# Kernel optimization log

Hardware: AMD Instinct MI355X
Metric: run time of the kernel (lower is better)

Reference implementation:

```python
import jax, jax.numpy as jnp
import numpy as np

DIM = 1024
NUM_EXPERTS = 8
NUM_SELECTED = 2
HIDDEN = 4096
B, S = 2, 2048


def setup_inputs() -> dict:
    key = jax.random.key(0)
    ks = jax.random.split(key, 12)
    scale = 0.02
    x = jax.random.normal(ks[0], (B, S, DIM), dtype=jnp.float32)
    router_w = jax.random.normal(ks[1], (DIM, NUM_EXPERTS), dtype=jnp.float32) * scale
    router_b = jnp.zeros((NUM_EXPERTS,), dtype=jnp.float32)
    w1 = jax.random.normal(ks[2], (NUM_EXPERTS, DIM, HIDDEN), dtype=jnp.float32) * scale
    b1 = jnp.zeros((NUM_EXPERTS, HIDDEN), dtype=jnp.float32)
    w2 = jax.random.normal(ks[3], (NUM_EXPERTS, HIDDEN, DIM), dtype=jnp.float32) * scale
    b2 = jnp.zeros((NUM_EXPERTS, DIM), dtype=jnp.float32)
    sw1 = jax.random.normal(ks[4], (DIM, HIDDEN), dtype=jnp.float32) * scale
    sb1 = jnp.zeros((HIDDEN,), dtype=jnp.float32)
    sw2 = jax.random.normal(ks[5], (HIDDEN, DIM), dtype=jnp.float32) * scale
    sb2 = jnp.zeros((DIM,), dtype=jnp.float32)
    return {"x": x, "router_w": router_w, "router_b": router_b,
            "w1": w1, "b1": b1, "w2": w2, "b2": b2,
            "sw1": sw1, "sb1": sb1, "sw2": sw2, "sb2": sb2}


def _ffn(x, wa, ba, wb, bb):
    # exact (erf) GELU, matching torch nn.GELU() default
    h = jax.nn.gelu(x @ wa + ba, approximate=False)
    return h @ wb + bb


def reference(x, router_w, router_b, w1, b1, w2, b2, sw1, sb1, sw2, sb2):
    # router: [B,S,E] softmax, then top-k over experts (eval mode: no noise)
    logits = x @ router_w + router_b
    probs = jax.nn.softmax(logits, axis=-1)
    top_w, top_i = jax.lax.top_k(probs, NUM_SELECTED)  # [B,S,K]
    # combine weights per expert: [B,S,E]; masked-out experts get weight 0,
    # so computing every expert densely and weighting is the same math as
    # the original masked-dispatch loop.
    combine = jnp.sum(top_w[..., None] * jax.nn.one_hot(top_i, NUM_EXPERTS, dtype=x.dtype), axis=-2)
    shared = _ffn(x, sw1, sb1, sw2, sb2)
    out = shared
    for e in range(NUM_EXPERTS):  # small fixed structural loop over experts
        out = out + combine[..., e:e + 1] * _ffn(x, w1[e], b1[e], w2[e], b2[e])
    return out
```

## Files before the change

### kernel.cpp

```cpp
#include <hip/hip_runtime.h>
#include <hip/hip_bf16.h>

#define T_TOK   4096
#define DIM     1024
#define NEXP    8
#define HID     4096
#define CAPPAD  9216
#define MTOT    (CAPPAD + T_TOK)
static_assert(MTOT % 128 == 0, "MTOT must be multiple of 128");

typedef __attribute__((ext_vector_type(8))) short bf16x8;
typedef __attribute__((ext_vector_type(4))) float f32x4;

typedef const __attribute__((address_space(1))) unsigned int* gas1_u32;
typedef __attribute__((address_space(3))) unsigned int* las3_u32;

__device__ __forceinline__ void async_ld16(const void* g, void* l) {
    __builtin_amdgcn_global_load_lds((gas1_u32)g, (las3_u32)l, 16, 0, 0);
}

__device__ __forceinline__ unsigned short f2bf(float f) {
    union { float f; unsigned u; } v; v.f = f;
    unsigned r = v.u + 0x7fffu + ((v.u >> 16) & 1u);
    return (unsigned short)(r >> 16);
}

__global__ __launch_bounds__(256)
void router_kernel(const float* __restrict__ x, const float* __restrict__ rw,
                   const float* __restrict__ rb, int* __restrict__ cnt,
                   int* __restrict__ top_e, float* __restrict__ top_w) {
    const int tid  = threadIdx.x;
    const int lane = tid & 63;
    const int t    = blockIdx.x * 4 + (tid >> 6);
    const float* xr = x + (size_t)t * DIM;
    float acc[NEXP];
#pragma unroll
    for (int e = 0; e < NEXP; ++e) acc[e] = 0.f;
    for (int d = lane; d < DIM; d += 64) {
        float xv = xr[d];
        const float* r = rw + (size_t)d * NEXP;
#pragma unroll
        for (int e = 0; e < NEXP; ++e) acc[e] += xv * r[e];
    }
#pragma unroll
    for (int off = 32; off > 0; off >>= 1) {
#pragma unroll
        for (int e = 0; e < NEXP; ++e) acc[e] += __shfl_down(acc[e], off);
    }
    if (lane == 0) {
        float lg[NEXP], p[NEXP];
        float mx = -1e30f;
#pragma unroll
        for (int e = 0; e < NEXP; ++e) { lg[e] = acc[e] + rb[e]; mx = fmaxf(mx, lg[e]); }
        float s = 0.f;
#pragma unroll
        for (int e = 0; e < NEXP; ++e) { p[e] = expf(lg[e] - mx); s += p[e]; }
        float inv = 1.f / s;
#pragma unroll
        for (int e = 0; e < NEXP; ++e) p[e] *= inv;
        int i1 = 0;
#pragma unroll
        for (int e = 1; e < NEXP; ++e) if (p[e] > p[i1]) i1 = e;
        int i2 = (i1 == 0) ? 1 : 0;
#pragma unroll
        for (int e = 0; e < NEXP; ++e) if (e != i1 && p[e] > p[i2]) i2 = e;
        top_e[2 * t]     = i1;  top_w[2 * t]     = p[i1];
        top_e[2 * t + 1] = i2;  top_w[2 * t + 1] = p[i2];
        atomicAdd(&cnt[i1], 1);
        atomicAdd(&cnt[i2], 1);
    }
}

__global__ void offsets_kernel(const int* __restrict__ cnt, int* __restrict__ poff) {
    if (threadIdx.x == 0) {
        int acc = 0;
#pragma unroll
        for (int e = 0; e < NEXP; ++e) { poff[e] = acc; acc += (cnt[e] + 127) & ~127; }
        poff[NEXP] = acc;
    }
}

__global__ __launch_bounds__(256)
void assign_kernel(const int* __restrict__ top_e, const int* __restrict__ poff,
                   int* __restrict__ cursor, int* __restrict__ slot_of,
                   int* __restrict__ rowtok) {
    int t = blockIdx.x * 256 + threadIdx.x;
#pragma unroll
    for (int k = 0; k < 2; ++k) {
        int e = top_e[2 * t + k];
        int s = poff[e] + atomicAdd(&cursor[e], 1);
        slot_of[2 * t + k] = s;
        rowtok[s] = t;
    }
}

__global__ __launch_bounds__(256)
void gather_kernel(const float* __restrict__ x, const int* __restrict__ rowtok,
                   unsigned short* __restrict__ xg) {
    int row = blockIdx.x;
    int t = (row >= CAPPAD) ? (row - CAPPAD) : rowtok[row];
    ushort4* dst = (ushort4*)(xg + (size_t)row * DIM) + threadIdx.x;
    if (t < 0) { ushort4 z; z.x = z.y = z.z = z.w = 0; *dst = z; return; }
    float4 v = ((const float4*)(x + (size_t)t * DIM))[threadIdx.x];
    ushort4 o; o.x = f2bf(v.x); o.y = f2bf(v.y); o.z = f2bf(v.z); o.w = f2bf(v.w);
    *dst = o;
}

__global__ __launch_bounds__(256)
void transpose_convert(const float* __restrict__ in, unsigned short* __restrict__ out,
                       int R, int C) {
    __shared__ float tile[64][65];
    const size_t bofs = (size_t)blockIdx.z * R * C;
    in += bofs; out += bofs;
    const int r0 = blockIdx.y * 64, c0 = blockIdx.x * 64;
    const int tc = threadIdx.x & 63, tr = threadIdx.x >> 6;
#pragma unroll
    for (int j = 0; j < 16; ++j)
        tile[tr + j * 4][tc] = in[(size_t)(r0 + tr + j * 4) * C + c0 + tc];
    __syncthreads();
#pragma unroll
    for (int j = 0; j < 16; ++j)
        out[(size_t)(c0 + tr + j * 4) * R + r0 + tc] = f2bf(tile[tc][tr + j * 4]);
}

template <int N, int K, bool GELU>
__global__ __launch_bounds__(256, 2)
void gemm_kernel(const unsigned short* __restrict__ A,
                 const unsigned short* __restrict__ Wt,
                 const unsigned short* __restrict__ SWt,
                 const float* __restrict__ Bias, const float* __restrict__ SBias,
                 const int* __restrict__ poff, void* __restrict__ Out) {
    __shared__ unsigned short As[128 * 64];
    __shared__ unsigned short Bs[128 * 64];
    const int tid = threadIdx.x, lane = tid & 63;
    const int wr = tid >> 7, wc = (tid >> 6) & 1;
    const int row0 = blockIdx.y * 128, col0 = blockIdx.x * 128;

    const unsigned short* Bt; const float* bias;
    if (row0 >= CAPPAD) { Bt = SWt; bias = SBias; }
    else {
        int e = 0;
#pragma unroll
        for (int i = 1; i < NEXP; ++i) e += (row0 >= poff[i]);
        Bt = Wt + (size_t)e * N * K; bias = Bias + (size_t)e * N;
    }

    f32x4 acc[4][4];
#pragma unroll
    for (int m = 0; m < 4; ++m)
#pragma unroll
        for (int n = 0; n < 4; ++n) acc[m][n] = (f32x4){0.f, 0.f, 0.f, 0.f};

    for (int kt = 0; kt < K / 64; ++kt) {
        const int kb = kt * 64;
#pragma unroll
        for (int j = 0; j < 4; ++j) {
            int c  = j * 256 + tid;
            int r  = c >> 3, k8 = c & 7;
            async_ld16(A  + (size_t)(row0 + r) * K + kb + k8 * 8, As + c * 8);
            async_ld16(Bt + (size_t)(col0 + r) * K + kb + k8 * 8, Bs + c * 8);
        }
        __syncthreads();
#pragma unroll
        for (int kk = 0; kk < 2; ++kk) {
            bf16x8 af[4], bfr[4];
#pragma unroll
            for (int m = 0; m < 4; ++m)
                af[m] = *(const bf16x8*)(As + (wr * 64 + m * 16 + (lane & 15)) * 64 + kk * 32 + (lane >> 4) * 8);
#pragma unroll
            for (int n = 0; n < 4; ++n)
                bfr[n] = *(const bf16x8*)(Bs + (wc * 64 + n * 16 + (lane & 15)) * 64 + kk * 32 + (lane >> 4) * 8);
#pragma unroll
            for (int m = 0; m < 4; ++m)
#pragma unroll
                for (int n = 0; n < 4; ++n)
                    acc[m][n] = __builtin_amdgcn_mfma_f32_16x16x32_bf16(af[m], bfr[n], acc[m][n], 0, 0, 0);
        }
        __syncthreads();
    }

    const int rb_ = row0 + wr * 64 + ((lane >> 4) << 2);
#pragma unroll
    for (int n = 0; n < 4; ++n) {
        const int col = col0 + wc * 64 + n * 16 + (lane & 15);
        const float bv = bias[col];
#pragma unroll
        for (int m = 0; m < 4; ++m) {
#pragma unroll
            for (int j = 0; j < 4; ++j) {
                const int row = rb_ + m * 16 + j;
                float v = acc[m][n][j] + bv;
                if (GELU) {
                    v = 0.5f * v * (1.f + erff(v * 0.70710678118654752f));
                    ((unsigned short*)Out)[(size_t)row * N + col] = f2bf(v);
                } else {
                    ((float*)Out)[(size_t)row * N + col] = v;
                }
            }
        }
    }
}

__global__ __launch_bounds__(256)
void combine_kernel(const float* __restrict__ Y, const int* __restrict__ slot_of,
                    const float* __restrict__ top_w, float* __restrict__ out) {
    const int t = blockIdx.x, i = threadIdx.x;
    const int s0 = slot_of[2 * t], s1 = slot_of[2 * t + 1];
    const float w0 = top_w[2 * t], w1 = top_w[2 * t + 1];
    float4 ys = ((const float4*)(Y + (size_t)(CAPPAD + t) * DIM))[i];
    float4 y0 = ((const float4*)(Y + (size_t)s0 * DIM))[i];
    float4 y1 = ((const float4*)(Y + (size_t)s1 * DIM))[i];
    float4 r;
    r.x = ys.x + w0 * y0.x + w1 * y1.x;
    r.y = ys.y + w0 * y0.y + w1 * y1.y;
    r.z = ys.z + w0 * y0.z + w1 * y1.z;
    r.w = ys.w + w0 * y0.w + w1 * y1.w;
    ((float4*)(out + (size_t)t * DIM))[i] = r;
}

extern "C" void kernel_launch(void* const* d_in, const int* in_sizes, int n_in,
                              void* d_out, int out_size, void* d_ws, size_t ws_size,
                              hipStream_t stream) {
    const float* x   = (const float*)d_in[0];
    const float* rw  = (const float*)d_in[1];
    const float* rb  = (const float*)d_in[2];
    const float* w1  = (const float*)d_in[3];
    const float* b1  = (const float*)d_in[4];
    const float* w2  = (const float*)d_in[5];
    const float* b2  = (const float*)d_in[6];
    const float* sw1 = (const float*)d_in[7];
    const float* sb1 = (const float*)d_in[8];
    const float* sw2 = (const float*)d_in[9];
    const float* sb2 = (const float*)d_in[10];
    float* out = (float*)d_out;

    char* ws = (char*)d_ws;
    size_t off = 0;
    auto alloc = [&](size_t bytes) {
        off = (off + 255) & ~(size_t)255;
        size_t p = off; off += bytes; return p;
    };
    int*   meta    = (int*)(ws + alloc(32 * sizeof(int)));
    int*   cnt     = meta;
    int*   cursor  = meta + 8;
    int*   poff    = meta + 16;
    int*   top_e   = (int*)  (ws + alloc((size_t)2 * T_TOK * 4));
    float* top_w   = (float*)(ws + alloc((size_t)2 * T_TOK * 4));
    int*   slot_of = (int*)  (ws + alloc((size_t)2 * T_TOK * 4));
    int*   rowtok  = (int*)  (ws + alloc((size_t)CAPPAD * 4));
    unsigned short* xg   = (unsigned short*)(ws + alloc((size_t)MTOT * DIM * 2));
    unsigned short* w1t  = (unsigned short*)(ws + alloc((size_t)NEXP * HID * DIM * 2));
    unsigned short* w2t  = (unsigned short*)(ws + alloc((size_t)NEXP * DIM * HID * 2));
    unsigned short* sw1t = (unsigned short*)(ws + alloc((size_t)HID * DIM * 2));
    unsigned short* sw2t = (unsigned short*)(ws + alloc((size_t)DIM * HID * 2));
    unsigned short* H    = (unsigned short*)(ws + alloc((size_t)MTOT * HID * 2));
    float*          Y    = (float*)         (ws + alloc((size_t)MTOT * DIM * 4));

    hipMemsetAsync(meta, 0, 16 * sizeof(int), stream);
    hipMemsetAsync(rowtok, 0xFF, (size_t)CAPPAD * 4, stream);

    transpose_convert<<<dim3(HID / 64, DIM / 64, NEXP), 256, 0, stream>>>(w1,  w1t,  DIM, HID);
    transpose_convert<<<dim3(DIM / 64, HID / 64, NEXP), 256, 0, stream>>>(w2,  w2t,  HID, DIM);
    transpose_convert<<<dim3(HID / 64, DIM / 64, 1),    256, 0, stream>>>(sw1, sw1t, DIM, HID);
    transpose_convert<<<dim3(DIM / 64, HID / 64, 1),    256, 0, stream>>>(sw2, sw2t, HID, DIM);

    router_kernel<<<T_TOK / 4, 256, 0, stream>>>(x, rw, rb, cnt, top_e, top_w);
    offsets_kernel<<<1, 64, 0, stream>>>(cnt, poff);
    assign_kernel<<<T_TOK / 256, 256, 0, stream>>>(top_e, poff, cursor, slot_of, rowtok);
    gather_kernel<<<MTOT, 256, 0, stream>>>(x, rowtok, xg);

    gemm_kernel<HID, DIM, true ><<<dim3(HID / 128, MTOT / 128), 256, 0, stream>>>(
        xg, w1t, sw1t, b1, sb1, poff, (void*)H);
    gemm_kernel<DIM, HID, false><<<dim3(DIM / 128, MTOT / 128), 256, 0, stream>>>(
        H, w2t, sw2t, b2, sb2, poff, (void*)Y);

    combine_kernel<<<T_TOK, 256, 0, stream>>>(Y, slot_of, top_w, out);
}
```

Measured before the change: 916.2 us.

## Rewrite expert GEMMs as 256x256 double-buffered tiles and vectorize weight transpose

Replaces the 128x128 single-buffered GEMM with a 512-thread 256x256 tile kernel. The new kernel double-buffers LDS, interleaves async prefetch with MFMA quarters, swizzles LDS to avoid bank conflicts, raises wave priority during MFMA, and remaps workgroups across XCDs. Expert capacity padding grows to multiples of 256, which adds some wasted rows. The weight transpose now uses 128x128 tiles with float4 loads and a swizzled bf16 LDS tile, and Y reuses the w1t buffer to save workspace. The larger tiles cut global and LDS traffic per FLOP but cost more registers and more padding.

```diff
diff --git a/kernel.cpp b/kernel.cpp
--- a/kernel.cpp
+++ b/kernel.cpp
@@ -5,9 +5,10 @@
 #define DIM     1024
 #define NEXP    8
 #define HID     4096
-#define CAPPAD  9216
+#define CAPPAD  10240
 #define MTOT    (CAPPAD + T_TOK)
-static_assert(MTOT % 128 == 0, "MTOT must be multiple of 128");
+static_assert(MTOT % 256 == 0, "MTOT must be multiple of 256");
+static_assert(CAPPAD % 256 == 0, "CAPPAD must be multiple of 256");
 
 typedef __attribute__((ext_vector_type(8))) short bf16x8;
 typedef __attribute__((ext_vector_type(4))) float f32x4;
@@ -23,6 +24,17 @@
     union { float f; unsigned u; } v; v.f = f;
     unsigned r = v.u + 0x7fffu + ((v.u >> 16) & 1u);
     return (unsigned short)(r >> 16);
+}
+
+#define BAR() do { asm volatile("" ::: "memory"); __builtin_amdgcn_s_barrier(); asm volatile("" ::: "memory"); } while (0)
+#define VMCNT4() asm volatile("s_waitcnt vmcnt(4)" ::: "memory")
+#define VMCNT2() asm volatile("s_waitcnt vmcnt(2)" ::: "memory")
+#define VMCNT0() asm volatile("s_waitcnt vmcnt(0)" ::: "memory")
+
+__device__ __forceinline__ int xcd_swizzle(int wg, int nwg) {
+    int q = nwg >> 3, r = nwg & 7;
+    int x = wg & 7, i = wg >> 3;
+    return (x < r ? x * (q + 1) : r * (q + 1) + (x - r) * q) + i;
 }
 
 __global__ __launch_bounds__(256)
@@ -75,7 +87,7 @@
     if (threadIdx.x == 0) {
         int acc = 0;
 #pragma unroll
-        for (int e = 0; e < NEXP; ++e) { poff[e] = acc; acc += (cnt[e] + 127) & ~127; }
+        for (int e = 0; e < NEXP; ++e) { poff[e] = acc; acc += (cnt[e] + 255) & ~255; }
         poff[NEXP] = acc;
     }
 }
@@ -109,32 +121,52 @@
 __global__ __launch_bounds__(256)
 void transpose_convert(const float* __restrict__ in, unsigned short* __restrict__ out,
                        int R, int C) {
-    __shared__ float tile[64][65];
+    __shared__ __align__(16) unsigned short tb[128][128];
     const size_t bofs = (size_t)blockIdx.z * R * C;
-    in += bofs; out += bofs;
-    const int r0 = blockIdx.y * 64, c0 = blockIdx.x * 64;
-    const int tc = threadIdx.x & 63, tr = threadIdx.x >> 6;
-#pragma unroll
-    for (int j = 0; j < 16; ++j)
-        tile[tr + j * 4][tc] = in[(size_t)(r0 + tr + j * 4) * C + c0 + tc];
+    const int r0 = blockIdx.y * 128, c0 = blockIdx.x * 128;
+    const int lr = threadIdx.x >> 5;
+    const int lc = threadIdx.x & 31;
+#pragma unroll
+    for (int s_ = 0; s_ < 16; ++s_) {
+        int r = s_ * 8 + lr;
+        float4 v = *(const float4*)&in[bofs + (size_t)(r0 + r) * C + c0 + lc * 4];
+        ushort4 o; o.x = f2bf(v.x); o.y = f2bf(v.y); o.z = f2bf(v.z); o.w = f2bf(v.w);
+        *(ushort4*)&tb[r][(lc * 4) ^ (r & 124)] = o;
+    }
     __syncthreads();
 #pragma unroll
-    for (int j = 0; j < 16; ++j)
-        out[(size_t)(c0 + tr + j * 4) * R + r0 + tc] = f2bf(tile[tc][tr + j * 4]);
+    for (int s_ = 0; s_ < 16; ++s_) {
+        int c = s_ * 8 + lr;
+        int rb_ = lc * 4;
+        ushort4 o;
+        o.x = tb[rb_ + 0][c ^ rb_];
+        o.y = tb[rb_ + 1][c ^ rb_];
+        o.z = tb[rb_ + 2][c ^ rb_];
+        o.w = tb[rb_ + 3][c ^ rb_];
+        *(ushort4*)&out[bofs + (size_t)(c0 + c) * R + r0 + rb_] = o;
+    }
 }
 
 template <int N, int K, bool GELU>
-__global__ __launch_bounds__(256, 2)
-void gemm_kernel(const unsigned short* __restrict__ A,
-                 const unsigned short* __restrict__ Wt,
-                 const unsigned short* __restrict__ SWt,
-                 const float* __restrict__ Bias, const float* __restrict__ SBias,
-                 const int* __restrict__ poff, void* __restrict__ Out) {
-    __shared__ unsigned short As[128 * 64];
-    __shared__ unsigned short Bs[128 * 64];
-    const int tid = threadIdx.x, lane = tid & 63;
-    const int wr = tid >> 7, wc = (tid >> 6) & 1;
-    const int row0 = blockIdx.y * 128, col0 = blockIdx.x * 128;
+__global__ __launch_bounds__(512, 2)
+void gemm256_kernel(const unsigned short* __restrict__ A,
+                    const unsigned short* __restrict__ Wt,
+                    const unsigned short* __restrict__ SWt,
+                    const float* __restrict__ Bias, const float* __restrict__ SBias,
+                    const int* __restrict__ poff, void* __restrict__ Out,
+                    int nwg, int ncol) {
+    __shared__ __align__(16) unsigned short As[2][2][128 * 64];
+    __shared__ __align__(16) unsigned short Bs[2][2][128 * 64];
+
+    const int tid  = threadIdx.x;
+    const int lane = tid & 63;
+    const int wid  = tid >> 6;
+    const int wr   = wid >> 2;
+    const int wc   = wid & 3;
+
+    const int wg  = xcd_swizzle(blockIdx.x, nwg);
+    const int bx  = wg % ncol, by = wg / ncol;
+    const int row0 = by * 256, col0 = bx * 256;
 
     const unsigned short* Bt; const float* bias;
     if (row0 >= CAPPAD) { Bt = SWt; bias = SBias; }
@@ -145,60 +177,142 @@
         Bt = Wt + (size_t)e * N * K; bias = Bias + (size_t)e * N;
     }
 
-    f32x4 acc[4][4];
-#pragma unroll
-    for (int m = 0; m < 4; ++m)
-#pragma unroll
-        for (int n = 0; n < 4; ++n) acc[m][n] = (f32x4){0.f, 0.f, 0.f, 0.f};
-
-    for (int kt = 0; kt < K / 64; ++kt) {
-        const int kb = kt * 64;
-#pragma unroll
-        for (int j = 0; j < 4; ++j) {
-            int c  = j * 256 + tid;
-            int r  = c >> 3, k8 = c & 7;
-            async_ld16(A  + (size_t)(row0 + r) * K + kb + k8 * 8, As + c * 8);
-            async_ld16(Bt + (size_t)(col0 + r) * K + kb + k8 * 8, Bs + c * 8);
+    constexpr int NT = K / 64;
+    static_assert(NT >= 2, "need >=2 k-tiles");
+
+    auto stage = [&](const unsigned short* gbase, unsigned short* lds) {
+#pragma unroll
+        for (int i = 0; i < 2; ++i) {
+            int c = i * 512 + tid;
+            int r = c >> 3;
+            int s = (c & 7) ^ (r & 7);
+            async_ld16(gbase + (size_t)r * K + s * 8, lds + c * 8);
         }
-        __syncthreads();
-#pragma unroll
-        for (int kk = 0; kk < 2; ++kk) {
-            bf16x8 af[4], bfr[4];
-#pragma unroll
-            for (int m = 0; m < 4; ++m)
-                af[m] = *(const bf16x8*)(As + (wr * 64 + m * 16 + (lane & 15)) * 64 + kk * 32 + (lane >> 4) * 8);
-#pragma unroll
-            for (int n = 0; n < 4; ++n)
-                bfr[n] = *(const bf16x8*)(Bs + (wc * 64 + n * 16 + (lane & 15)) * 64 + kk * 32 + (lane >> 4) * 8);
-#pragma unroll
-            for (int m = 0; m < 4; ++m)
-#pragma unroll
-                for (int n = 0; n < 4; ++n)
-                    acc[m][n] = __builtin_amdgcn_mfma_f32_16x16x32_bf16(af[m], bfr[n], acc[m][n], 0, 0, 0);
-        }
-        __syncthreads();
-    }
-
-    const int rb_ = row0 + wr * 64 + ((lane >> 4) << 2);
-#pragma unroll
-    for (int n = 0; n < 4; ++n) {
-        const int col = col0 + wc * 64 + n * 16 + (lane & 15);
-        const float bv = bias[col];
-#pragma unroll
-        for (int m = 0; m < 4; ++m) {
-#pragma unroll
-            for (int j = 0; j < 4; ++j) {
-                const int row = rb_ + m * 16 + j;
-                float v = acc[m][n][j] + bv;
-                if (GELU) {
-                    v = 0.5f * v * (1.f + erff(v * 0.70710678118654752f));
-                    ((unsigned short*)Out)[(size_t)row * N + col] = f2bf(v);
-                } else {
-                    ((float*)Out)[(size_t)row * N + col] = v;
+    };
+
+    f32x4 acc[2][2][4][2];
+#pragma unroll
+    for (int a0 = 0; a0 < 2; ++a0)
+#pragma unroll
+        for (int a1 = 0; a1 < 2; ++a1)
+#pragma unroll
+            for (int a2 = 0; a2 < 4; ++a2)
+#pragma unroll
+                for (int a3 = 0; a3 < 2; ++a3) acc[a0][a1][a2][a3] = (f32x4){0.f, 0.f, 0.f, 0.f};
+
+    bf16x8 af[4][2];
+    bf16x8 bf0[2][2], bf1[2][2];
+
+    auto lda = [&](int b, int mh, int mp, int kk) -> bf16x8 {
+        int r = wr * 64 + mp * 16 + (lane & 15);
+        int q = kk * 4 + (lane >> 4);
+        return *(const bf16x8*)&As[b][mh][r * 64 + ((q ^ (r & 7)) * 8)];
+    };
+    auto ldb = [&](int b, int nh, int np, int kk) -> bf16x8 {
+        int r = wc * 32 + np * 16 + (lane & 15);
+        int q = kk * 4 + (lane >> 4);
+        return *(const bf16x8*)&Bs[b][nh][r * 64 + ((q ^ (r & 7)) * 8)];
+    };
+
+    stage(A  + (size_t)(row0 +   0) * K, &As[0][0][0]);
+    stage(Bt + (size_t)(col0 +   0) * K, &Bs[0][0][0]);
+    stage(Bt + (size_t)(col0 + 128) * K, &Bs[0][1][0]);
+    stage(A  + (size_t)(row0 + 128) * K, &As[0][1][0]);
+    VMCNT4();
+    BAR();
+
+    for (int t = 0; t < NT; ++t) {
+        const int b  = t & 1;
+        const bool pf = (t + 1 < NT);
+        const int kb1 = (t + 1) * 64;
+
+#pragma unroll
+        for (int mp = 0; mp < 4; ++mp) { af[mp][0] = lda(b, 0, mp, 0); af[mp][1] = lda(b, 0, mp, 1); }
+#pragma unroll
+        for (int np = 0; np < 2; ++np) { bf0[np][0] = ldb(b, 0, np, 0); bf0[np][1] = ldb(b, 0, np, 1); }
+        if (pf) stage(A + (size_t)(row0 + 0) * K + kb1, &As[b ^ 1][0][0]);
+        BAR();
+        __builtin_amdgcn_s_setprio(1);
+#pragma unroll
+        for (int kk = 0; kk < 2; ++kk)
+#pragma unroll
+            for (int mp = 0; mp < 4; ++mp)
+#pragma unroll
+                for (int np = 0; np < 2; ++np)
+                    acc[0][0][mp][np] = __builtin_amdgcn_mfma_f32_16x16x32_bf16(af[mp][kk], bf0[np][kk], acc[0][0][mp][np], 0, 0, 0);
+        __builtin_amdgcn_s_setprio(0);
+        if (pf) VMCNT4(); else VMCNT2();
+        BAR();
+
+#pragma unroll
+        for (int np = 0; np < 2; ++np) { bf1[np][0] = ldb(b, 1, np, 0); bf1[np][1] = ldb(b, 1, np, 1); }
+        if (pf) stage(Bt + (size_t)(col0 + 0) * K + kb1, &Bs[b ^ 1][0][0]);
+        BAR();
+        __builtin_amdgcn_s_setprio(1);
+#pragma unroll
+        for (int kk = 0; kk < 2; ++kk)
+#pragma unroll
+            for (int mp = 0; mp < 4; ++mp)
+#pragma unroll
+                for (int np = 0; np < 2; ++np)
+                    acc[0][1][mp][np] = __builtin_amdgcn_mfma_f32_16x16x32_bf16(af[mp][kk], bf1[np][kk], acc[0][1][mp][np], 0, 0, 0);
+        __builtin_amdgcn_s_setprio(0);
+        if (pf) VMCNT4(); else VMCNT0();
+        BAR();
+
+#pragma unroll
+        for (int mp = 0; mp < 4; ++mp) { af[mp][0] = lda(b, 1, mp, 0); af[mp][1] = lda(b, 1, mp, 1); }
+        if (pf) stage(Bt + (size_t)(col0 + 128) * K + kb1, &Bs[b ^ 1][1][0]);
+        BAR();
+        __builtin_amdgcn_s_setprio(1);
+#pragma unroll
+        for (int kk = 0; kk < 2; ++kk)
+#pragma unroll
+            for (int mp = 0; mp < 4; ++mp)
+#pragma unroll
+                for (int np = 0; np < 2; ++np)
+                    acc[1][1][mp][np] = __builtin_amdgcn_mfma_f32_16x16x32_bf16(af[mp][kk], bf1[np][kk], acc[1][1][mp][np], 0, 0, 0);
+        __builtin_amdgcn_s_setprio(0);
+        BAR();
+
+        if (pf) stage(A + (size_t)(row0 + 128) * K + kb1, &As[b ^ 1][1][0]);
+        BAR();
+        __builtin_amdgcn_s_setprio(1);
+#pragma unroll
+        for (int kk = 0; kk < 2; ++kk)
+#pragma unroll
+            for (int mp = 0; mp < 4; ++mp)
+#pragma unroll
+                for (int np = 0; np < 2; ++np)
+                    acc[1][0][mp][np] = __builtin_amdgcn_mfma_f32_16x16x32_bf16(af[mp][kk], bf0[np][kk], acc[1][0][mp][np], 0, 0, 0);
+        __builtin_amdgcn_s_setprio(0);
+        if (pf) VMCNT4();
+        BAR();
+    }
+
+#pragma unroll
+    for (int mh = 0; mh < 2; ++mh)
+#pragma unroll
+        for (int nh = 0; nh < 2; ++nh)
+#pragma unroll
+            for (int np = 0; np < 2; ++np) {
+                const int col = col0 + nh * 128 + wc * 32 + np * 16 + (lane & 15);
+                const float bv = bias[col];
+#pragma unroll
+                for (int mp = 0; mp < 4; ++mp) {
+#pragma unroll
+                    for (int j = 0; j < 4; ++j) {
+                        const int row = row0 + mh * 128 + wr * 64 + mp * 16 + ((lane >> 4) << 2) + j;
+                        float v = acc[mh][nh][mp][np][j] + bv;
+                        if (GELU) {
+                            v = 0.5f * v * (1.f + erff(v * 0.70710678118654752f));
+                            ((unsigned short*)Out)[(size_t)row * N + col] = f2bf(v);
+                        } else {
+                            ((float*)Out)[(size_t)row * N + col] = v;
+                        }
+                    }
                 }
             }
-        }
-    }
 }
 
 __global__ __launch_bounds__(256)
@@ -249,30 +363,37 @@
     int*   slot_of = (int*)  (ws + alloc((size_t)2 * T_TOK * 4));
     int*   rowtok  = (int*)  (ws + alloc((size_t)CAPPAD * 4));
     unsigned short* xg   = (unsigned short*)(ws + alloc((size_t)MTOT * DIM * 2));
-    unsigned short* w1t  = (unsigned short*)(ws + alloc((size_t)NEXP * HID * DIM * 2));
+    size_t w1t_off = alloc((size_t)NEXP * HID * DIM * 2);
+    unsigned short* w1t  = (unsigned short*)(ws + w1t_off);
     unsigned short* w2t  = (unsigned short*)(ws + alloc((size_t)NEXP * DIM * HID * 2));
     unsigned short* sw1t = (unsigned short*)(ws + alloc((size_t)HID * DIM * 2));
     unsigned short* sw2t = (unsigned short*)(ws + alloc((size_t)DIM * HID * 2));
     unsigned short* H    = (unsigned short*)(ws + alloc((size_t)MTOT * HID * 2));
-    float*          Y    = (float*)         (ws + alloc((size_t)MTOT * DIM * 4));
+    float*          Y    = (float*)(ws + w1t_off);
 
     hipMemsetAsync(meta, 0, 16 * sizeof(int), stream);
     hipMemsetAsync(rowtok, 0xFF, (size_t)CAPPAD * 4, stream);
 
-    transpose_convert<<<dim3(HID / 64, DIM / 64, NEXP), 256, 0, stream>>>(w1,  w1t,  DIM, HID);
-    transpose_convert<<<dim3(DIM / 64, HID / 64, NEXP), 256, 0, stream>>>(w2,  w2t,  HID, DIM);
-    transpose_convert<<<dim3(HID / 64, DIM / 64, 1),    256, 0, stream>>>(sw1, sw1t, DIM, HID);
-    transpose_convert<<<dim3(DIM / 64, HID / 64, 1),    256, 0, stream>>>(sw2, sw2t, HID, DIM);
+    transpose_convert<<<dim3(HID / 128, DIM / 128, NEXP), 256, 0, stream>>>(w1,  w1t,  DIM, HID);
+    transpose_convert<<<dim3(DIM / 128, HID / 128, NEXP), 256, 0, stream>>>(w2,  w2t,  HID, DIM);
+    transpose_convert<<<dim3(HID / 128, DIM / 128, 1),    256, 0, stream>>>(sw1, sw1t, DIM, HID);
+    transpose_convert<<<dim3(DIM / 128, HID / 128, 1),    256, 0, stream>>>(sw2, sw2t, HID, DIM);
 
     router_kernel<<<T_TOK / 4, 256, 0, stream>>>(x, rw, rb, cnt, top_e, top_w);
     offsets_kernel<<<1, 64, 0, stream>>>(cnt, poff);
     assign_kernel<<<T_TOK / 256, 256, 0, stream>>>(top_e, poff, cursor, slot_of, rowtok);
     gather_kernel<<<MTOT, 256, 0, stream>>>(x, rowtok, xg);
 
-    gemm_kernel<HID, DIM, true ><<<dim3(HID / 128, MTOT / 128), 256, 0, stream>>>(
-        xg, w1t, sw1t, b1, sb1, poff, (void*)H);
-    gemm_kernel<DIM, HID, false><<<dim3(DIM / 128, MTOT / 128), 256, 0, stream>>>(
-        H, w2t, sw2t, b2, sb2, poff, (void*)Y);
+    {
+        const int ncol = HID / 256, nwg = ncol * (MTOT / 256);
+        gemm256_kernel<HID, DIM, true><<<nwg, 512, 0, stream>>>(
+            xg, w1t, sw1t, b1, sb1, poff, (void*)H, nwg, ncol);
+    }
+    {
+        const int ncol = DIM / 256, nwg = ncol * (MTOT / 256);
+        gemm256_kernel<DIM, HID, false><<<nwg, 512, 0, stream>>>(
+            H, w2t, sw2t, b2, sb2, poff, (void*)Y, nwg, ncol);
+    }
 
     combine_kernel<<<T_TOK, 256, 0, stream>>>(Y, slot_of, top_w, out);
 }
```

Measured after the change: 880.5 us. -3.9%, faster.
